# Optimization experiments

Hardware: AMD Instinct MI355X
Metric: run time of the kernel (lower is better)

The kernel has to match this reference:

```python
import jax, jax.numpy as jnp
import numpy as np
from jax import lax

B, H, W = 32, 30, 30          # batch of ARC-style grids (max 30x30)
D, NH = 256, 4                # hidden_dim, num_heads (ARPSConfig)
L, P = 8, 12                  # max_program_length, number of primitives
NUM_COLORS = 10
PAINT_COLOR = 3


def setup_inputs() -> dict:
    key = jax.random.key(0)
    ks = jax.random.split(key, 11)
    s = 0.02
    return {
        "grid": jax.random.randint(ks[0], (B, H, W), 0, NUM_COLORS, dtype=jnp.int32),
        "anchor": jax.random.randint(ks[1], (B, 2), 0, min(H, W), dtype=jnp.int32),
        "embed": jax.random.normal(ks[2], (NUM_COLORS, D), jnp.float32) * s,
        "pos_emb": jax.random.normal(ks[3], (H * W, D), jnp.float32) * s,
        "wq": jax.random.normal(ks[4], (D, D), jnp.float32) * s,
        "wk": jax.random.normal(ks[5], (D, D), jnp.float32) * s,
        "wv": jax.random.normal(ks[6], (D, D), jnp.float32) * s,
        "wo": jax.random.normal(ks[7], (D, D), jnp.float32) * s,
        "step_q": jax.random.normal(ks[8], (L, D), jnp.float32) * s,
        "w_out": jax.random.normal(ks[9], (D, P), jnp.float32) * s,
        "b_out": jnp.zeros((P,), jnp.float32),
    }


def _mha(q, k, v, nh):
    b, lq, d = q.shape
    hd = d // nh
    qh = q.reshape(b, lq, nh, hd)
    kh = k.reshape(b, k.shape[1], nh, hd)
    vh = v.reshape(b, v.shape[1], nh, hd)
    scores = jnp.einsum('bqhd,bkhd->bhqk', qh, kh) / jnp.sqrt(jnp.asarray(hd, q.dtype))
    attn = jax.nn.softmax(scores, axis=-1)
    return jnp.einsum('bhqk,bkhd->bqhd', attn, vh).reshape(b, lq, d)


def _execute_one(grid, anchor):
    """Fixed anchor-relative program: select_connected((0,0)) -> rotate_90 -> paint."""
    h, w = grid.shape
    ar = jnp.clip(anchor[0], 0, h - 1)
    ac = jnp.clip(anchor[1], 0, w - 1)
    # --- select_connected: 4-connected component of seed color (parallel flood fill) ---
    seed_color = grid[ar, ac]
    same = grid == seed_color
    m0 = jnp.zeros((h, w), bool).at[ar, ac].set(True)

    def dilate(m):
        p = jnp.pad(m, 1)
        return m | p[:-2, 1:-1] | p[2:, 1:-1] | p[1:-1, :-2] | p[1:-1, 2:]

    def body(st):
        m = st[0]
        nm = dilate(m) & same
        return (nm, jnp.any(nm != m))

    mask, _ = lax.while_loop(lambda st: st[1], body, (m0, jnp.array(True)))
    sel = mask.astype(jnp.float32)
    # --- rotate_90 clockwise around anchor: (dr,dc) -> (dc,-dr); out-of-bounds dropped ---
    rr = jnp.broadcast_to(jnp.arange(h)[:, None], (h, w))
    cc = jnp.broadcast_to(jnp.arange(w)[None, :], (h, w))
    nr = ar + (cc - ac)
    nc = ac - (rr - ar)
    rot = jnp.zeros_like(sel).at[nr, nc].set(sel, mode='drop')
    # --- paint: overwrite selected pixels with PAINT_COLOR ---
    return jnp.where(rot > 0.5, jnp.int32(PAINT_COLOR), grid)


def reference(grid, anchor, embed, pos_emb, wq, wk, wv, wo, step_q, w_out, b_out):
    b = grid.shape[0]
    tok = embed[grid.reshape(b, -1)] + pos_emb                  # (B, T=900, D)
    tok = tok + _mha(tok @ wq, tok @ wk, tok @ wv, NH) @ wo     # self-attn over pixels
    sq = jnp.broadcast_to(step_q, (b,) + step_q.shape)          # (B, L, D) step queries
    hsteps = _mha(sq @ wq, tok @ wk, tok @ wv, NH) @ wo         # cross-attn: steps -> pixels
    logits = hsteps @ w_out + b_out                             # (B, L, P) primitive logits
    out_grid = jax.vmap(_execute_one)(grid, anchor)             # (B, H, W) executed program
    return logits, out_grid
```

## Files before the change

kernel.cpp:

```cpp
#include <hip/hip_runtime.h>


typedef __attribute__((ext_vector_type(8))) short bf16x8;
typedef __attribute__((ext_vector_type(4))) float f32x4;

constexpr float kScl = 0.18033688011112042f;

__device__ __forceinline__ short f2bf(float f) {
  union { float f; unsigned u; } v; v.f = f;
  unsigned r = v.u + 0x7fffu + ((v.u >> 16) & 1u);
  return (short)(r >> 16);
}
__device__ __forceinline__ float bf2f(short s) {
  union { unsigned u; float f; } v; v.u = ((unsigned)(unsigned short)s) << 16;
  return v.f;
}
__device__ __forceinline__ unsigned cvt_pk_bf16(float lo, float hi) {
  unsigned r;
  asm("v_cvt_pk_bf16_f32 %0, %1, %2" : "=v"(r) : "v"(lo), "v"(hi));
  return r;
}
__device__ __forceinline__ float exp2f_fast(float x) {
  return __builtin_amdgcn_exp2f(x);
}
__device__ __forceinline__ int swz(int row, int col) {
  return row * 64 + ((((col >> 3) ^ row) & 7) << 3) + (col & 7);
}
__device__ __forceinline__ int a256(int row, int col) {
  return row * 256 + (col & ~63) + (((((col >> 3) & 7) ^ row) & 7) << 3);
}
__device__ __forceinline__ void gload16(const short* gsrc, short* lds) {
  __builtin_amdgcn_global_load_lds(
      (const __attribute__((address_space(1))) unsigned int*)gsrc,
      (__attribute__((address_space(3))) unsigned int*)lds, 16, 0, 0);
}

constexpr size_t OFF_POSQ  = 0;
constexpr size_t OFF_POSK  = 230400;
constexpr size_t OFF_POSV  = 460800;
constexpr size_t OFF_EMBQ  = 691200;
constexpr size_t OFF_EMBK  = 693760;
constexpr size_t OFF_EMBV  = 696320;
constexpr size_t OFF_WOOUT = 698880;
constexpr size_t OFF_Q2    = 701952;
constexpr size_t OFF_QP    = 704000;
constexpr size_t OFF_QE    = OFF_QP + 28800;
constexpr size_t OFF_WVO   = OFF_QE + 512;
constexpr size_t OFF_Q2K   = OFF_WVO + 12288;
constexpr size_t OFF_F32_END = 769536;
constexpr size_t SOFF_WOKVT = 0;
constexpr size_t SOFF_ATTN  = 131072;
constexpr size_t SOFF_KB    = 7503872;
constexpr size_t SOFF_VT    = 14876672;
constexpr size_t SOFF_E     = SOFF_KB;
constexpr size_t SOFF_UPART = SOFF_KB + 983040;
constexpr size_t SOFF_VPART = SOFF_UPART + 2097152;

__global__ __launch_bounds__(256) void k_pre(const float* __restrict__ pos_emb,
                                             const float* __restrict__ embed,
                                             const float* __restrict__ wq,
                                             const float* __restrict__ wk,
                                             const float* __restrict__ wv,
                                             const float* __restrict__ wo,
                                             const float* __restrict__ step_q,
                                             const float* __restrict__ w_out,
                                             float* __restrict__ ws) {
  const int blk = blockIdx.x;
  const int tid = threadIdx.x;
  if (blk >= 212) {
    const int b2 = blk - 212;
    int job, base;
    if      (b2 < 10) { job = 0; base = b2; }
    else if (b2 < 20) { job = 1; base = b2 - 10; }
    else if (b2 < 30) { job = 2; base = b2 - 20; }
    else if (b2 < 42) { job = 3; base = b2 - 30; }
    else              { job = 4; base = b2 - 42; }
    const float* A; const float* Wm; float* C; int M; int N;
    switch (job) {
      case 0: A=embed;  Wm=wq;    C=ws+OFF_EMBQ;  M=10;  N=256; break;
      case 1: A=embed;  Wm=wk;    C=ws+OFF_EMBK;  M=10;  N=256; break;
      case 2: A=embed;  Wm=wv;    C=ws+OFF_EMBV;  M=10;  N=256; break;
      case 3: A=wo;     Wm=w_out; C=ws+OFF_WOOUT; M=256; N=12;  break;
      default:A=step_q; Wm=wq;    C=ws+OFF_Q2;    M=8;   N=256; break;
    }
    int idx = base * 256 + tid;
    if (idx >= M * N) return;
    int m = idx / N, n = idx - m * N;
    const float* a = A + (size_t)m * 256;
    float acc = 0.f;
    #pragma unroll 8
    for (int k = 0; k < 256; ++k) acc = fmaf(a[k], Wm[(size_t)k * N + n], acc);
    C[idx] = acc;
    return;
  }

  bool wojob; int mt, n0, base_n = 0;
  const float* A; const float* W; float* C = nullptr;
  if (blk < 180) {
    wojob = false; mt = blk % 15; int nt = blk / 15;
    A = pos_emb;
    W = nt < 4 ? wq : (nt < 8 ? wk : wv);
    C = ws + (nt < 4 ? OFF_POSQ : (nt < 8 ? OFF_POSK : OFF_POSV));
    n0 = (nt & 3) * 64;
  } else {
    wojob = true; int j = blk - 180; mt = j & 3; int nt2 = j >> 2;
    A = wo;
    W = nt2 < 4 ? wk : wv;
    base_n = nt2 < 4 ? 0 : 256;
    n0 = (nt2 & 3) * 64;
  }
  const int m0 = mt * 64;
  const int tr = tid >> 4, tc = tid & 15;
  __shared__ float As[64][68];
  __shared__ float Bs[64][68];
  float acc[4][4] = {};
  for (int kc = 0; kc < 4; ++kc) {
    __syncthreads();
    for (int i = tid; i < 1024; i += 256) {
      int row = i >> 4, c4 = (i & 15) * 4;
      int m = m0 + row; if (m > 899) m = 899;
      *(float4*)&As[row][c4] = *(const float4*)&A[(size_t)m * 256 + kc * 64 + c4];
      *(float4*)&Bs[row][c4] = *(const float4*)&W[(size_t)(kc * 64 + row) * 256 + n0 + c4];
    }
    __syncthreads();
    #pragma unroll 8
    for (int kk = 0; kk < 64; ++kk) {
      float a0 = As[4*tr+0][kk], a1 = As[4*tr+1][kk];
      float a2 = As[4*tr+2][kk], a3 = As[4*tr+3][kk];
      float4 b4 = *(const float4*)&Bs[kk][4*tc];
      acc[0][0]+=a0*b4.x; acc[0][1]+=a0*b4.y; acc[0][2]+=a0*b4.z; acc[0][3]+=a0*b4.w;
      acc[1][0]+=a1*b4.x; acc[1][1]+=a1*b4.y; acc[1][2]+=a1*b4.z; acc[1][3]+=a1*b4.w;
      acc[2][0]+=a2*b4.x; acc[2][1]+=a2*b4.y; acc[2][2]+=a2*b4.z; acc[2][3]+=a2*b4.w;
      acc[3][0]+=a3*b4.x; acc[3][1]+=a3*b4.y; acc[3][2]+=a3*b4.z; acc[3][3]+=a3*b4.w;
    }
  }
  if (!wojob) {
    #pragma unroll
    for (int i = 0; i < 4; ++i) {
      int m = m0 + 4 * tr + i;
      if (m < 900)
        *(float4*)&C[(size_t)m * 256 + n0 + 4 * tc] =
            make_float4(acc[i][0], acc[i][1], acc[i][2], acc[i][3]);
    }
  } else {
    __syncthreads();
    #pragma unroll
    for (int i = 0; i < 4; ++i)
      #pragma unroll
      for (int j = 0; j < 4; ++j)
        Bs[4 * tc + j][4 * tr + i] = acc[i][j];
    __syncthreads();
    short* wokvT = (short*)(ws + OFF_F32_END) + SOFF_WOKVT;
    for (int i = tid; i < 512; i += 256) {
      int row = i >> 3, ch = i & 7;
      union { short s[8]; bf16x8 v; } u;
      #pragma unroll
      for (int jj = 0; jj < 8; ++jj) u.s[jj] = f2bf(Bs[row][ch * 8 + jj]);
      *(bf16x8*)&wokvT[(size_t)(base_n + n0 + row) * 256 + m0 + ch * 8] = u.v;
    }
  }
}

__global__ __launch_bounds__(256) void k_pre2(float* __restrict__ ws) {
  const float* q2 = ws + OFF_Q2;
  const short* wokvT = (const short*)(ws + OFF_F32_END) + SOFF_WOKVT;
  const int blk = blockIdx.x, tid = threadIdx.x;
  if (blk < 32) {
    int lh = blk, h = lh >> 3, l = lh & 7;
    __shared__ float qs[64];
    if (tid < 64) qs[tid] = q2[l * 256 + h * 64 + tid];
    __syncthreads();
    float acc = 0.f;
    for (int dd = 0; dd < 64; ++dd)
      acc = fmaf(qs[dd], bf2f(wokvT[(size_t)(h * 64 + dd) * 256 + tid]), acc);
    ((short*)(ws + OFF_Q2K))[lh * 256 + tid] = f2bf(acc);
  } else if (blk < 64) {
    int lh = blk - 32, h = lh >> 3, l = lh & 7;
    __shared__ float qs[64];
    if (tid < 64) qs[tid] = q2[l * 256 + h * 64 + tid];
    __syncthreads();
    const float* posK = ws + OFF_POSK;
    for (int t = tid; t < 900; t += 256) {
      float acc = 0.f;
      const float* pr = posK + (size_t)t * 256 + h * 64;
      #pragma unroll 8
      for (int dd = 0; dd < 64; ++dd) acc = fmaf(qs[dd], pr[dd], acc);
      ws[OFF_QP + (size_t)lh * 900 + t] = acc;
    }
  } else if (blk == 64) {
    const float* embK = ws + OFF_EMBK;
    if (tid < 320) {
      int lh = tid / 10, c = tid - lh * 10;
      int h = lh >> 3, l = lh & 7;
      float acc = 0.f;
      const float* qrow = q2 + l * 256 + h * 64;
      const float* er = embK + (size_t)c * 256 + h * 64;
      for (int dd = 0; dd < 64; ++dd) acc = fmaf(qrow[dd], er[dd], acc);
      ws[OFF_QE + lh * 16 + c] = acc;
    }
  } else {
    int h = blk - 65;
    const float* woOut = ws + OFF_WOOUT;
    __shared__ float wos[64][12];
    for (int i = tid; i < 768; i += 256) wos[i / 12][i % 12] = woOut[(h * 64 + i / 12) * 12 + i % 12];
    __syncthreads();
    float acc[12] = {};
    for (int dd = 0; dd < 64; ++dd) {
      float v = bf2f(wokvT[(size_t)(256 + h * 64 + dd) * 256 + tid]);
      #pragma unroll
      for (int p = 0; p < 12; ++p) acc[p] = fmaf(v, wos[dd][p], acc[p]);
    }
    #pragma unroll
    for (int p = 0; p < 12; ++p)
      ws[OFF_WVO + ((size_t)h * 256 + tid) * 12 + p] = acc[p];
  }
}

__global__ __launch_bounds__(256) void k_kv(const int* __restrict__ grid_in,
                                            const float* __restrict__ ws,
                                            short* __restrict__ Kb,
                                            short* __restrict__ VT) {
  const int kt = blockIdx.x, b = blockIdx.y;
  const int t0 = kt * 64, tid = threadIdx.x;
  const float* posK = ws + OFF_POSK;
  const float* embK = ws + OFF_EMBK;
  const float* posV = ws + OFF_POSV;
  const float* embV = ws + OFF_EMBV;

  for (int i = tid; i < 2048; i += 256) {
    int row = i >> 5, ch = i & 31;
    int t = t0 + row;
    if (t > 899) continue;
    int g = grid_in[b * 900 + t];
    const float* pk = posK + (size_t)t * 256 + ch * 8;
    const float* ek = embK + (size_t)g * 256 + ch * 8;
    float4 p0 = *(const float4*)pk, p1 = *(const float4*)(pk + 4);
    float4 e0 = *(const float4*)ek, e1 = *(const float4*)(ek + 4);
    union { short s[8]; bf16x8 v; } u;
    u.s[0] = f2bf(p0.x + e0.x); u.s[1] = f2bf(p0.y + e0.y);
    u.s[2] = f2bf(p0.z + e0.z); u.s[3] = f2bf(p0.w + e0.w);
    u.s[4] = f2bf(p1.x + e1.x); u.s[5] = f2bf(p1.y + e1.y);
    u.s[6] = f2bf(p1.z + e1.z); u.s[7] = f2bf(p1.w + e1.w);
    *(bf16x8*)&Kb[((size_t)(b * 900 + t)) * 256 + ch * 8] = u.v;
  }

  __shared__ float Lf[64 * 65];
  for (int h = 0; h < 4; ++h) {
    __syncthreads();
    for (int i = tid; i < 512; i += 256) {
      int row = i >> 3, ch = i & 7;
      int t = t0 + row; if (t > 899) t = 899;
      int g = grid_in[b * 900 + t];
      const float* pv = posV + (size_t)t * 256 + h * 64 + ch * 8;
      const float* ev = embV + (size_t)g * 256 + h * 64 + ch * 8;
      float4 p0 = *(const float4*)pv, p1 = *(const float4*)(pv + 4);
      float4 e0 = *(const float4*)ev, e1 = *(const float4*)(ev + 4);
      float* L = &Lf[row * 65 + ch * 8];
      L[0] = p0.x + e0.x; L[1] = p0.y + e0.y; L[2] = p0.z + e0.z; L[3] = p0.w + e0.w;
      L[4] = p1.x + e1.x; L[5] = p1.y + e1.y; L[6] = p1.z + e1.z; L[7] = p1.w + e1.w;
    }
    __syncthreads();
    short* tile = VT + ((size_t)((b * 4 + h) * 15 + kt)) * 4096;
    #pragma unroll
    for (int u = 0; u < 2; ++u) {
      int unit = u * 256 + tid;
      int d = unit >> 3;
      int t8 = (unit & 7) * 8;
      union { short s[8]; bf16x8 v; } p;
      #pragma unroll
      for (int i = 0; i < 8; ++i) p.s[i] = f2bf(Lf[(t8 + i) * 65 + d]);
      *(bf16x8*)&tile[d * 64 + t8] = p.v;
    }
  }
}

__global__ __launch_bounds__(256) void k_attn(const int* __restrict__ grid_in,
                                              const float* __restrict__ ws,
                                              const short* __restrict__ Kb,
                                              const short* __restrict__ VT,
                                              short* __restrict__ attnOut) {
  const int bidx = blockIdx.x;
  const int bh = ((bidx >> 6) << 3) | (bidx & 7);
  const int qt = (bidx >> 3) & 7;
  const int h = bh & 3, b = bh >> 2;
  const int t0 = qt * 128, hc = h * 64;
  const int tid = threadIdx.x, w = tid >> 6, lane = tid & 63;
  const int g = lane >> 4, c16 = lane & 15;
  const size_t tileBase = (size_t)(bh * 15) * 4096;

  __shared__ __align__(16) short Ks[2][4096];
  __shared__ __align__(16) short Vs[2][4096];
  __shared__ __align__(16) short Ps[4096];

  const float* posQ = ws + OFF_POSQ;
  const float* embQ = ws + OFF_EMBQ;

  bf16x8 aQ[2][2];
  #pragma unroll
  for (int s = 0; s < 2; ++s) {
    int t = t0 + s * 64 + w * 16 + c16; if (t > 899) t = 899;
    int gq = grid_in[b * 900 + t];
    #pragma unroll
    for (int kc = 0; kc < 2; ++kc) {
      union { short s8[8]; bf16x8 v; } u;
      #pragma unroll
      for (int j = 0; j < 8; ++j) {
        int d = hc + kc * 32 + g * 8 + j;
        u.s8[j] = f2bf(kScl * (embQ[gq * 256 + d] + posQ[(size_t)t * 256 + d]));
      }
      aQ[s][kc] = u.v;
    }
  }

#define STAGE(BUF, KT)                                                        \
  do {                                                                        \
    int kk0_ = (KT) * 64;                                                     \
    _Pragma("unroll")                                                         \
    for (int j_ = 0; j_ < 2; ++j_) {                                          \
      int c_ = j_ * 256 + w * 64 + lane;                                      \
      int row_ = c_ >> 3, ch_ = c_ & 7;                                       \
      int t_ = kk0_ + row_; if (t_ > 899) t_ = 899;                           \
      int sw_ = ((ch_ ^ row_) & 7) << 3;                                      \
      gload16(Kb + ((size_t)(b * 900 + t_)) * 256 + hc + sw_,                 \
              &Ks[BUF][(j_ * 256 + w * 64) << 3]);                            \
      gload16(VT + tileBase + (size_t)(KT) * 4096 + (row_ << 6) + sw_,        \
              &Vs[BUF][(j_ * 256 + w * 64) << 3]);                            \
    }                                                                         \
  } while (0)

  float l_[2] = {0.f, 0.f};
  f32x4 O[2][4];
  #pragma unroll
  for (int s = 0; s < 2; ++s)
    #pragma unroll
    for (int dt = 0; dt < 4; ++dt) { f32x4 z = {0.f,0.f,0.f,0.f}; O[s][dt] = z; }

  STAGE(0, 0);
  __syncthreads();

  int cur = 0;
  for (int kt = 0; kt < 15; ++kt) {
    if (kt + 1 < 15) STAGE(cur ^ 1, kt + 1);

    if (kt < 14) {
      f32x4 sacc[2][4];
      #pragma unroll
      for (int ct = 0; ct < 4; ++ct) {
        bf16x8 aK0 = *(bf16x8*)&Ks[cur][swz(ct * 16 + c16, g * 8)];
        bf16x8 aK1 = *(bf16x8*)&Ks[cur][swz(ct * 16 + c16, 32 + g * 8)];
        #pragma unroll
        for (int s = 0; s < 2; ++s) {
          f32x4 z = {0.f, 0.f, 0.f, 0.f};
          z = __builtin_amdgcn_mfma_f32_16x16x32_bf16(aK0, aQ[s][0], z, 0, 0, 0);
          z = __builtin_amdgcn_mfma_f32_16x16x32_bf16(aK1, aQ[s][1], z, 0, 0, 0);
          sacc[s][ct] = z;
        }
      }
      #pragma unroll
      for (int s = 0; s < 2; ++s) {
        float rs = 0.f;
        unsigned pk[4][2];
        #pragma unroll
        for (int ct = 0; ct < 4; ++ct) {
          float p0 = exp2f_fast(sacc[s][ct][0]);
          float p1 = exp2f_fast(sacc[s][ct][1]);
          float p2 = exp2f_fast(sacc[s][ct][2]);
          float p3 = exp2f_fast(sacc[s][ct][3]);
          rs += (p0 + p1) + (p2 + p3);
          pk[ct][0] = cvt_pk_bf16(p0, p1);
          pk[ct][1] = cvt_pk_bf16(p2, p3);
        }
        rs += __shfl_xor(rs, 16);
        rs += __shfl_xor(rs, 32);
        l_[s] += rs;
        #pragma unroll
        for (int ct = 0; ct < 4; ++ct)
          *(uint2*)&Ps[swz(w * 16 + c16, ct * 16 + 4 * g)] =
              make_uint2(pk[ct][0], pk[ct][1]);
        #pragma unroll
        for (int c = 0; c < 2; ++c) {
          bf16x8 aP = *(bf16x8*)&Ps[swz(w * 16 + c16, c * 32 + g * 8)];
          #pragma unroll
          for (int dt = 0; dt < 4; ++dt) {
            bf16x8 bV = *(bf16x8*)&Vs[cur][swz(dt * 16 + c16, c * 32 + g * 8)];
            O[s][dt] = __builtin_amdgcn_mfma_f32_16x16x32_bf16(aP, bV, O[s][dt], 0, 0, 0);
          }
        }
      }
    } else {
      bf16x8 aK0 = *(bf16x8*)&Ks[cur][swz(c16, g * 8)];
      bf16x8 aK1 = *(bf16x8*)&Ks[cur][swz(c16, 32 + g * 8)];
      #pragma unroll
      for (int s = 0; s < 2; ++s) {
        f32x4 z = {0.f, 0.f, 0.f, 0.f};
        z = __builtin_amdgcn_mfma_f32_16x16x32_bf16(aK0, aQ[s][0], z, 0, 0, 0);
        z = __builtin_amdgcn_mfma_f32_16x16x32_bf16(aK1, aQ[s][1], z, 0, 0, 0);
        float p0 = 0.f, p1 = 0.f, p2 = 0.f, p3 = 0.f;
        if (g == 0) {
          p0 = exp2f_fast(z[0]); p1 = exp2f_fast(z[1]);
          p2 = exp2f_fast(z[2]); p3 = exp2f_fast(z[3]);
        }
        float rs = (p0 + p1) + (p2 + p3);
        rs += __shfl_xor(rs, 16);
        rs += __shfl_xor(rs, 32);
        l_[s] += rs;
        *(uint2*)&Ps[swz(w * 16 + c16, 4 * g)] =
            make_uint2(cvt_pk_bf16(p0, p1), cvt_pk_bf16(p2, p3));
        *(uint2*)&Ps[swz(w * 16 + c16, 16 + 4 * g)] = make_uint2(0u, 0u);
        bf16x8 aP = *(bf16x8*)&Ps[swz(w * 16 + c16, g * 8)];
        #pragma unroll
        for (int dt = 0; dt < 4; ++dt) {
          bf16x8 bV = *(bf16x8*)&Vs[cur][swz(dt * 16 + c16, g * 8)];
          O[s][dt] = __builtin_amdgcn_mfma_f32_16x16x32_bf16(aP, bV, O[s][dt], 0, 0, 0);
        }
      }
    }

    __syncthreads();
    cur ^= 1;
  }
#undef STAGE

  #pragma unroll
  for (int s = 0; s < 2; ++s) {
    #pragma unroll
    for (int r = 0; r < 4; ++r) {
      float lq = __shfl(l_[s], (g << 4) | (4 * g + r));
      int t = t0 + s * 64 + w * 16 + 4 * g + r;
      if (t < 900) {
        float inv = 1.f / lq;
        #pragma unroll
        for (int dt = 0; dt < 4; ++dt)
          attnOut[((size_t)(b * 900 + t)) * 256 + hc + dt * 16 + c16] =
              f2bf(O[s][dt][r] * inv);
      }
    }
  }
}

__global__ __launch_bounds__(256) void k_crossA(const int* __restrict__ grid_in,
                                                const float* __restrict__ ws,
                                                const short* __restrict__ attnOut,
                                                short* __restrict__ E,
                                                float* __restrict__ Sp) {
  const int kt = blockIdx.x, b = blockIdx.y;
  const int t0 = kt * 64;
  const int tid = threadIdx.x, w = tid >> 6, lane = tid & 63;
  const int g = lane >> 4, c16 = lane & 15;
  __shared__ __align__(16) short Aat[16384];
  __shared__ __align__(16) short Qk[8192];
  __shared__ float qpL[32 * 72];
  __shared__ float qeL[512];
  __shared__ int   gtl[64];
  __shared__ float spW[128];

  #pragma unroll
  for (int it = 0; it < 8; ++it) {
    int idx = it * 256 + w * 64 + lane;
    int row = idx >> 5, ch = idx & 31;
    int t = t0 + row; if (t > 899) t = 899;
    int sw = (((ch & 7) ^ row) & 7) << 3;
    gload16(attnOut + ((size_t)(b * 900 + t)) * 256 + (ch >> 3) * 64 + sw,
            &Aat[(it * 256 + w * 64) << 3]);
  }
  const short* q2k = (const short*)(ws + OFF_Q2K);
  #pragma unroll
  for (int it = 0; it < 4; ++it) {
    int idx = it * 256 + w * 64 + lane;
    int row = idx >> 5, ch = idx & 31;
    int sw = (((ch & 7) ^ row) & 7) << 3;
    gload16(q2k + (size_t)row * 256 + (ch >> 3) * 64 + sw,
            &Qk[(it * 256 + w * 64) << 3]);
  }
  #pragma unroll
  for (int it = 0; it < 2; ++it) {
    int idx = it * 256 + tid, row = idx >> 4, c4 = (idx & 15) * 4;
    *(float4*)&qpL[row * 72 + c4] = *(const float4*)&ws[OFF_QP + (size_t)row * 900 + t0 + c4];
  }
  for (int idx = tid; idx < 512; idx += 256) qeL[idx] = ws[OFF_QE + idx];
  if (tid < 64) { int t = t0 + tid; gtl[tid] = grid_in[b * 900 + (t > 899 ? 899 : t)]; }
  __syncthreads();

  f32x4 sacc[2];
  { f32x4 z = {0.f,0.f,0.f,0.f}; sacc[0] = z; sacc[1] = z; }
  #pragma unroll
  for (int kk = 0; kk < 8; ++kk) {
    bf16x8 aA = *(bf16x8*)&Aat[a256(w * 16 + c16, kk * 32 + g * 8)];
    bf16x8 b0 = *(bf16x8*)&Qk[a256(c16, kk * 32 + g * 8)];
    bf16x8 b1 = *(bf16x8*)&Qk[a256(16 + c16, kk * 32 + g * 8)];
    sacc[0] = __builtin_amdgcn_mfma_f32_16x16x32_bf16(aA, b0, sacc[0], 0, 0, 0);
    sacc[1] = __builtin_amdgcn_mfma_f32_16x16x32_bf16(aA, b1, sacc[1], 0, 0, 0);
  }
  #pragma unroll
  for (int ct = 0; ct < 2; ++ct) {
    int lh = ct * 16 + c16;
    float e[4]; float rs = 0.f;
    #pragma unroll
    for (int r = 0; r < 4; ++r) {
      int tl = w * 16 + g * 4 + r;
      float s = kScl * (sacc[ct][r] + qpL[lh * 72 + tl] + qeL[lh * 16 + gtl[tl]]);
      e[r] = (t0 + tl < 900) ? exp2f_fast(s) : 0.f;
      rs += e[r];
    }
    *(uint2*)&E[((size_t)(b * 32 + lh)) * 960 + t0 + w * 16 + g * 4] =
        make_uint2(cvt_pk_bf16(e[0], e[1]), cvt_pk_bf16(e[2], e[3]));
    rs += __shfl_xor(rs, 16);
    rs += __shfl_xor(rs, 32);
    if (g == 0) spW[w * 32 + lh] = rs;
  }
  __syncthreads();
  if (tid < 32)
    Sp[((size_t)b * 32 + tid) * 15 + kt] =
        spW[tid] + spW[32 + tid] + spW[64 + tid] + spW[96 + tid];
}

__global__ __launch_bounds__(256) void k_crossP(const short* __restrict__ attnOut,
                                                const short* __restrict__ E,
                                                const short* __restrict__ VT,
                                                short* __restrict__ Upart,
                                                short* __restrict__ Vpart) {
  const int ktg = blockIdx.x, b = blockIdx.y;
  const int tid = threadIdx.x, w = tid >> 6, lane = tid & 63;
  const int g = lane >> 4, c16 = lane & 15;
  const int h = w, ctv = h >> 1;
  __shared__ __align__(16) short AT[256 * 72];
  __shared__ __align__(16) short Et[2048];
  __shared__ __align__(16) short VTl[16384];

  f32x4 Uacc[2][4], Vacc[4];
  { f32x4 z = {0.f,0.f,0.f,0.f};
    #pragma unroll
    for (int a = 0; a < 2; ++a)
      #pragma unroll
      for (int q = 0; q < 4; ++q) Uacc[a][q] = z;
    #pragma unroll
    for (int a = 0; a < 4; ++a) Vacc[a] = z; }

  const int ntile = (ktg < 7) ? 2 : 1;
  for (int tt = 0; tt < ntile; ++tt) {
    const int kt = ktg * 2 + tt, t0 = kt * 64;
    if (tt) __syncthreads();
    #pragma unroll
    for (int it = 0; it < 8; ++it) {
      int idx = it * 256 + tid;
      int tl = idx >> 5, jc = idx & 31;
      int t = t0 + tl; if (t > 899) t = 899;
      bf16x8 v = *(const bf16x8*)&attnOut[((size_t)(b * 900 + t)) * 256 + jc * 8];
      #pragma unroll
      for (int ii = 0; ii < 8; ++ii)
        AT[(jc * 8 + ii) * 72 + ((((tl >> 3) ^ jc) & 7) << 3) + (tl & 7)] = v[ii];
    }
    {
      int idx = w * 64 + lane;
      int row = idx >> 3, ch = idx & 7;
      int sw = ((ch ^ row) & 7) << 3;
      gload16(E + ((size_t)(b * 32 + row)) * 960 + t0 + sw, &Et[(w * 64) << 3]);
    }
    #pragma unroll
    for (int it = 0; it < 8; ++it) {
      int idx = it * 256 + w * 64 + lane;
      int hh = idx >> 9, rem = idx & 511;
      int row = rem >> 3, ch = rem & 7;
      int sw = ((ch ^ row) & 7) << 3;
      gload16(VT + ((size_t)((b * 4 + hh) * 15 + kt)) * 4096 + row * 64 + sw,
              &VTl[(it * 256 + w * 64) << 3]);
    }
    __syncthreads();
    #pragma unroll
    for (int kk = 0; kk < 2; ++kk) {
      bf16x8 aE0 = *(bf16x8*)&Et[swz(c16, kk * 32 + g * 8)];
      bf16x8 aE1 = *(bf16x8*)&Et[swz(16 + c16, kk * 32 + g * 8)];
      #pragma unroll
      for (int q = 0; q < 4; ++q) {
        int j = (w * 4 + q) * 16 + c16;
        int tch = kk * 4 + g;
        bf16x8 bA = *(bf16x8*)&AT[j * 72 + (((tch ^ (j >> 3)) & 7) << 3)];
        Uacc[0][q] = __builtin_amdgcn_mfma_f32_16x16x32_bf16(aE0, bA, Uacc[0][q], 0, 0, 0);
        Uacc[1][q] = __builtin_amdgcn_mfma_f32_16x16x32_bf16(aE1, bA, Uacc[1][q], 0, 0, 0);
      }
      bf16x8 bE = (ctv == 0) ? aE0 : aE1;
      #pragma unroll
      for (int rt = 0; rt < 4; ++rt) {
        bf16x8 aV = *(bf16x8*)&VTl[h * 4096 + swz(rt * 16 + c16, kk * 32 + g * 8)];
        Vacc[rt] = __builtin_amdgcn_mfma_f32_16x16x32_bf16(aV, bE, Vacc[rt], 0, 0, 0);
      }
    }
  }
  #pragma unroll
  for (int rt = 0; rt < 2; ++rt)
    #pragma unroll
    for (int q = 0; q < 4; ++q) {
      int j = (w * 4 + q) * 16 + c16;
      #pragma unroll
      for (int r = 0; r < 4; ++r) {
        int lh = rt * 16 + g * 4 + r;
        Upart[(((size_t)(ktg * 32 + b)) * 32 + lh) * 256 + j] = f2bf(Uacc[rt][q][r]);
      }
    }
  if ((c16 >> 3) == (h & 1)) {
    int l = c16 & 7;
    #pragma unroll
    for (int rt = 0; rt < 4; ++rt)
      #pragma unroll
      for (int r = 0; r < 4; ++r) {
        int d = rt * 16 + g * 4 + r;
        Vpart[((((size_t)(ktg * 32 + b)) * 4 + h) * 64 + d) * 8 + l] = f2bf(Vacc[rt][r]);
      }
  }
}

__global__ void k_crossR(const float* __restrict__ ws,
                         const float* __restrict__ b_out,
                         const short* __restrict__ Upart,
                         const short* __restrict__ Vpart,
                         const float* __restrict__ Sp,
                         float* __restrict__ out) {
  const int bl = blockIdx.x, b = bl >> 3, l = bl & 7;
  const int tid = threadIdx.x;
  __shared__ float Us[4][256];
  __shared__ float Vsm[4][64];
  __shared__ float Sinv[4];
  __shared__ float part[4][12];
  for (int h = 0; h < 4; ++h) {
    int lh = h * 8 + l;
    for (int j = tid; j < 256; j += 64) {
      float a = 0.f;
      #pragma unroll
      for (int kg = 0; kg < 8; ++kg)
        a += bf2f(Upart[(((size_t)(kg * 32 + b)) * 32 + lh) * 256 + j]);
      Us[h][j] = a;
    }
    float a = 0.f;
    #pragma unroll
    for (int kg = 0; kg < 8; ++kg)
      a += bf2f(Vpart[((((size_t)(kg * 32 + b)) * 4 + h) * 64 + tid) * 8 + l]);
    Vsm[h][tid] = a;
  }
  if (tid < 4) {
    int lh = tid * 8 + l;
    float s = 0.f;
    #pragma unroll
    for (int k = 0; k < 15; ++k) s += Sp[((size_t)b * 32 + lh) * 15 + k];
    Sinv[tid] = 1.f / s;
  }
  __syncthreads();
  if (tid < 48) {
    int h = tid / 12, p = tid % 12;
    const float* woOut = ws + OFF_WOOUT;
    const float* WVO = ws + OFF_WVO;
    float acc = 0.f;
    for (int dd = 0; dd < 64; ++dd)
      acc = fmaf(Vsm[h][dd], woOut[(h * 64 + dd) * 12 + p], acc);
    for (int j = 0; j < 256; ++j)
      acc = fmaf(Us[h][j], WVO[((size_t)h * 256 + j) * 12 + p], acc);
    part[h][p] = acc * Sinv[h];
  }
  __syncthreads();
  if (tid < 12)
    out[(size_t)bl * 12 + tid] =
        b_out[tid] + part[0][tid] + part[1][tid] + part[2][tid] + part[3][tid];
}

__global__ void k_execute(const int* __restrict__ grid_in,
                          const int* __restrict__ anchor,
                          float* __restrict__ outg) {
  const int b = blockIdx.x;
  const int lane = threadIdx.x;
  const int* g = grid_in + b * 900;
  int ar = anchor[2 * b], ac = anchor[2 * b + 1];
  ar = min(max(ar, 0), 29); ac = min(max(ac, 0), 29);
  const int seed = g[ar * 30 + ac];

  unsigned same = 0u;
  if (lane < 30)
    for (int c = 0; c < 30; ++c) same |= (unsigned)(g[lane * 30 + c] == seed) << c;

  unsigned cur = (lane == ar) ? (1u << ac) : 0u;
  bool changed = true;
  while (changed) {
    unsigned up = __shfl(cur, (lane + 63) & 63);
    unsigned dn = __shfl(cur, (lane + 1) & 63);
    if (lane == 0) up = 0u;
    unsigned nm = (cur | (cur << 1) | (cur >> 1) | up | dn) & same;
    changed = __any(nm != cur);
    cur = nm;
  }

  __shared__ unsigned msh[32];
  if (lane < 32) msh[lane] = (lane < 30) ? cur : 0u;
  __syncthreads();

  if (lane < 30) {
    unsigned rot = 0u;
    int cc = lane - ar + ac;
    if (cc >= 0 && cc < 30) {
      for (int nc = 0; nc < 30; ++nc) {
        int rr = ar + ac - nc;
        if (rr >= 0 && rr < 30) rot |= ((msh[rr] >> cc) & 1u) << nc;
      }
    }
    for (int c = 0; c < 30; ++c) {
      int v = ((rot >> c) & 1u) ? 3 : g[lane * 30 + c];
      outg[b * 900 + lane * 30 + c] = (float)v;
    }
  }
}

extern "C" void kernel_launch(void* const* d_in, const int* in_sizes, int n_in,
                              void* d_out, int out_size, void* d_ws, size_t ws_size,
                              hipStream_t stream) {
  const int*   grid_in = (const int*)d_in[0];
  const int*   anchor  = (const int*)d_in[1];
  const float* embed   = (const float*)d_in[2];
  const float* pos_emb = (const float*)d_in[3];
  const float* wq      = (const float*)d_in[4];
  const float* wk      = (const float*)d_in[5];
  const float* wv      = (const float*)d_in[6];
  const float* wo      = (const float*)d_in[7];
  const float* step_q  = (const float*)d_in[8];
  const float* w_out   = (const float*)d_in[9];
  const float* b_out   = (const float*)d_in[10];
  float* out = (float*)d_out;
  float* ws  = (float*)d_ws;
  short* wsS = (short*)(ws + OFF_F32_END);

  k_pre<<<dim3(262), dim3(256), 0, stream>>>(pos_emb, embed, wq, wk, wv, wo,
                                             step_q, w_out, ws);
  k_pre2<<<dim3(69), dim3(256), 0, stream>>>(ws);
  k_kv<<<dim3(15, 32), dim3(256), 0, stream>>>(grid_in, ws,
                                               wsS + SOFF_KB, wsS + SOFF_VT);
  k_attn<<<dim3(1024), dim3(256), 0, stream>>>(grid_in, ws, wsS + SOFF_KB,
                                               wsS + SOFF_VT, wsS + SOFF_ATTN);
  short* E  = wsS + SOFF_E;
  float* Sp = (float*)(wsS + SOFF_WOKVT);
  k_crossA<<<dim3(15, 32), dim3(256), 0, stream>>>(grid_in, ws, wsS + SOFF_ATTN, E, Sp);
  k_crossP<<<dim3(8, 32), dim3(256), 0, stream>>>(wsS + SOFF_ATTN, E, wsS + SOFF_VT,
                                                  wsS + SOFF_UPART, wsS + SOFF_VPART);
  k_crossR<<<dim3(256), dim3(64), 0, stream>>>(ws, b_out, wsS + SOFF_UPART,
                                               wsS + SOFF_VPART, Sp, out);
  k_execute<<<dim3(32), dim3(64), 0, stream>>>(grid_in, anchor, out + 32 * 8 * 12);
}
```

Before: 226.6 us.

## Merge launches for pre2/kv and crossR/execute; batch PV MFMAs with priority hints

```diff
diff --git a/kernel.cpp b/kernel.cpp
--- a/kernel.cpp
+++ b/kernel.cpp
@@ -161,67 +161,72 @@
   }
 }
 
-__global__ __launch_bounds__(256) void k_pre2(float* __restrict__ ws) {
-  const float* q2 = ws + OFF_Q2;
-  const short* wokvT = (const short*)(ws + OFF_F32_END) + SOFF_WOKVT;
+__global__ __launch_bounds__(256) void k_kvp(const int* __restrict__ grid_in,
+                                             float* __restrict__ ws,
+                                             short* __restrict__ Kb,
+                                             short* __restrict__ VT) {
   const int blk = blockIdx.x, tid = threadIdx.x;
-  if (blk < 32) {
-    int lh = blk, h = lh >> 3, l = lh & 7;
-    __shared__ float qs[64];
-    if (tid < 64) qs[tid] = q2[l * 256 + h * 64 + tid];
-    __syncthreads();
-    float acc = 0.f;
-    for (int dd = 0; dd < 64; ++dd)
-      acc = fmaf(qs[dd], bf2f(wokvT[(size_t)(h * 64 + dd) * 256 + tid]), acc);
-    ((short*)(ws + OFF_Q2K))[lh * 256 + tid] = f2bf(acc);
-  } else if (blk < 64) {
-    int lh = blk - 32, h = lh >> 3, l = lh & 7;
-    __shared__ float qs[64];
-    if (tid < 64) qs[tid] = q2[l * 256 + h * 64 + tid];
-    __syncthreads();
-    const float* posK = ws + OFF_POSK;
-    for (int t = tid; t < 900; t += 256) {
+  __shared__ float Lf[64 * 65];
+
+  if (blk >= 480) {
+    const int b2 = blk - 480;
+    const float* q2 = ws + OFF_Q2;
+    const short* wokvT = (const short*)(ws + OFF_F32_END) + SOFF_WOKVT;
+    if (b2 < 32) {
+      int lh = b2, h = lh >> 3, l = lh & 7;
+      float* qs = Lf;
+      if (tid < 64) qs[tid] = q2[l * 256 + h * 64 + tid];
+      __syncthreads();
       float acc = 0.f;
-      const float* pr = posK + (size_t)t * 256 + h * 64;
-      #pragma unroll 8
-      for (int dd = 0; dd < 64; ++dd) acc = fmaf(qs[dd], pr[dd], acc);
-      ws[OFF_QP + (size_t)lh * 900 + t] = acc;
-    }
-  } else if (blk == 64) {
-    const float* embK = ws + OFF_EMBK;
-    if (tid < 320) {
-      int lh = tid / 10, c = tid - lh * 10;
-      int h = lh >> 3, l = lh & 7;
-      float acc = 0.f;
-      const float* qrow = q2 + l * 256 + h * 64;
-      const float* er = embK + (size_t)c * 256 + h * 64;
-      for (int dd = 0; dd < 64; ++dd) acc = fmaf(qrow[dd], er[dd], acc);
-      ws[OFF_QE + lh * 16 + c] = acc;
-    }
-  } else {
-    int h = blk - 65;
-    const float* woOut = ws + OFF_WOOUT;
-    __shared__ float wos[64][12];
-    for (int i = tid; i < 768; i += 256) wos[i / 12][i % 12] = woOut[(h * 64 + i / 12) * 12 + i % 12];
-    __syncthreads();
-    float acc[12] = {};
-    for (int dd = 0; dd < 64; ++dd) {
-      float v = bf2f(wokvT[(size_t)(256 + h * 64 + dd) * 256 + tid]);
-      #pragma unroll
-      for (int p = 0; p < 12; ++p) acc[p] = fmaf(v, wos[dd][p], acc[p]);
-    }
-    #pragma unroll
-    for (int p = 0; p < 12; ++p)
-      ws[OFF_WVO + ((size_t)h * 256 + tid) * 12 + p] = acc[p];
-  }
-}
-
-__global__ __launch_bounds__(256) void k_kv(const int* __restrict__ grid_in,
-                                            const float* __restrict__ ws,
-                                            short* __restrict__ Kb,
-                                            short* __restrict__ VT) {
-  const int kt = blockIdx.x, b = blockIdx.y;
-  const int t0 = kt * 64, tid = threadIdx.x;
+      for (int dd = 0; dd < 64; ++dd)
+        acc = fmaf(qs[dd], bf2f(wokvT[(size_t)(h * 64 + dd) * 256 + tid]), acc);
+      ((short*)(ws + OFF_Q2K))[lh * 256 + tid] = f2bf(acc);
+    } else if (b2 < 64) {
+      int lh = b2 - 32, h = lh >> 3, l = lh & 7;
+      float* qs = Lf;
+      if (tid < 64) qs[tid] = q2[l * 256 + h * 64 + tid];
+      __syncthreads();
+      const float* posK = ws + OFF_POSK;
+      for (int t = tid; t < 900; t += 256) {
+        float acc = 0.f;
+        const float* pr = posK + (size_t)t * 256 + h * 64;
+        #pragma unroll 8
+        for (int dd = 0; dd < 64; ++dd) acc = fmaf(qs[dd], pr[dd], acc);
+        ws[OFF_QP + (size_t)lh * 900 + t] = acc;
+      }
+    } else if (b2 == 64) {
+      const float* embK = ws + OFF_EMBK;
+      if (tid < 320) {
+        int lh = tid / 10, c = tid - lh * 10;
+        int h = lh >> 3, l = lh & 7;
+        float acc = 0.f;
+        const float* qrow = q2 + l * 256 + h * 64;
+        const float* er = embK + (size_t)c * 256 + h * 64;
+        for (int dd = 0; dd < 64; ++dd) acc = fmaf(qrow[dd], er[dd], acc);
+        ws[OFF_QE + lh * 16 + c] = acc;
+      }
+    } else {
+      int h = b2 - 65;
+      const float* woOut = ws + OFF_WOOUT;
+      float (*wos)[12] = (float(*)[12])Lf;
+      for (int i = tid; i < 768; i += 256)
+        wos[i / 12][i % 12] = woOut[(h * 64 + i / 12) * 12 + i % 12];
+      __syncthreads();
+      float acc[12] = {};
+      for (int dd = 0; dd < 64; ++dd) {
+        float v = bf2f(wokvT[(size_t)(256 + h * 64 + dd) * 256 + tid]);
+        #pragma unroll
+        for (int p = 0; p < 12; ++p) acc[p] = fmaf(v, wos[dd][p], acc[p]);
+      }
+      #pragma unroll
+      for (int p = 0; p < 12; ++p)
+        ws[OFF_WVO + ((size_t)h * 256 + tid) * 12 + p] = acc[p];
+    }
+    return;
+  }
+
+  const int kt = blk % 15, b = blk / 15;
+  const int t0 = kt * 64;
   const float* posK = ws + OFF_POSK;
   const float* embK = ws + OFF_EMBK;
   const float* posV = ws + OFF_POSV;
@@ -244,7 +249,6 @@
     *(bf16x8*)&Kb[((size_t)(b * 900 + t)) * 256 + ch * 8] = u.v;
   }
 
-  __shared__ float Lf[64 * 65];
   for (int h = 0; h < 4; ++h) {
     __syncthreads();
     for (int i = tid; i < 512; i += 256) {
@@ -290,7 +294,7 @@
 
   __shared__ __align__(16) short Ks[2][4096];
   __shared__ __align__(16) short Vs[2][4096];
-  __shared__ __align__(16) short Ps[4096];
+  __shared__ __align__(16) short Ps[2][4096];
 
   const float* posQ = ws + OFF_POSQ;
   const float* embQ = ws + OFF_EMBQ;
@@ -344,6 +348,7 @@
 
     if (kt < 14) {
       f32x4 sacc[2][4];
+      __builtin_amdgcn_s_setprio(1);
       #pragma unroll
       for (int ct = 0; ct < 4; ++ct) {
         bf16x8 aK0 = *(bf16x8*)&Ks[cur][swz(ct * 16 + c16, g * 8)];
@@ -356,6 +361,7 @@
           sacc[s][ct] = z;
         }
       }
+      __builtin_amdgcn_s_setprio(0);
       #pragma unroll
       for (int s = 0; s < 2; ++s) {
         float rs = 0.f;
@@ -375,18 +381,22 @@
         l_[s] += rs;
         #pragma unroll
         for (int ct = 0; ct < 4; ++ct)
-          *(uint2*)&Ps[swz(w * 16 + c16, ct * 16 + 4 * g)] =
+          *(uint2*)&Ps[s][swz(w * 16 + c16, ct * 16 + 4 * g)] =
               make_uint2(pk[ct][0], pk[ct][1]);
+      }
+      __builtin_amdgcn_s_setprio(1);
+      #pragma unroll
+      for (int c = 0; c < 2; ++c) {
+        bf16x8 aP0 = *(bf16x8*)&Ps[0][swz(w * 16 + c16, c * 32 + g * 8)];
+        bf16x8 aP1 = *(bf16x8*)&Ps[1][swz(w * 16 + c16, c * 32 + g * 8)];
         #pragma unroll
-        for (int c = 0; c < 2; ++c) {
-          bf16x8 aP = *(bf16x8*)&Ps[swz(w * 16 + c16, c * 32 + g * 8)];
-          #pragma unroll
-          for (int dt = 0; dt < 4; ++dt) {
-            bf16x8 bV = *(bf16x8*)&Vs[cur][swz(dt * 16 + c16, c * 32 + g * 8)];
-            O[s][dt] = __builtin_amdgcn_mfma_f32_16x16x32_bf16(aP, bV, O[s][dt], 0, 0, 0);
-          }
+        for (int dt = 0; dt < 4; ++dt) {
+          bf16x8 bV = *(bf16x8*)&Vs[cur][swz(dt * 16 + c16, c * 32 + g * 8)];
+          O[0][dt] = __builtin_amdgcn_mfma_f32_16x16x32_bf16(aP0, bV, O[0][dt], 0, 0, 0);
+          O[1][dt] = __builtin_amdgcn_mfma_f32_16x16x32_bf16(aP1, bV, O[1][dt], 0, 0, 0);
         }
       }
+      __builtin_amdgcn_s_setprio(0);
     } else {
       bf16x8 aK0 = *(bf16x8*)&Ks[cur][swz(c16, g * 8)];
       bf16x8 aK1 = *(bf16x8*)&Ks[cur][swz(c16, 32 + g * 8)];
@@ -404,15 +414,17 @@
         rs += __shfl_xor(rs, 16);
         rs += __shfl_xor(rs, 32);
         l_[s] += rs;
-        *(uint2*)&Ps[swz(w * 16 + c16, 4 * g)] =
+        *(uint2*)&Ps[s][swz(w * 16 + c16, 4 * g)] =
             make_uint2(cvt_pk_bf16(p0, p1), cvt_pk_bf16(p2, p3));
-        *(uint2*)&Ps[swz(w * 16 + c16, 16 + 4 * g)] = make_uint2(0u, 0u);
-        bf16x8 aP = *(bf16x8*)&Ps[swz(w * 16 + c16, g * 8)];
-        #pragma unroll
-        for (int dt = 0; dt < 4; ++dt) {
-          bf16x8 bV = *(bf16x8*)&Vs[cur][swz(dt * 16 + c16, g * 8)];
-          O[s][dt] = __builtin_amdgcn_mfma_f32_16x16x32_bf16(aP, bV, O[s][dt], 0, 0, 0);
-        }
+        *(uint2*)&Ps[s][swz(w * 16 + c16, 16 + 4 * g)] = make_uint2(0u, 0u);
+      }
+      bf16x8 aP0 = *(bf16x8*)&Ps[0][swz(w * 16 + c16, g * 8)];
+      bf16x8 aP1 = *(bf16x8*)&Ps[1][swz(w * 16 + c16, g * 8)];
+      #pragma unroll
+      for (int dt = 0; dt < 4; ++dt) {
+        bf16x8 bV = *(bf16x8*)&Vs[cur][swz(dt * 16 + c16, g * 8)];
+        O[0][dt] = __builtin_amdgcn_mfma_f32_16x16x32_bf16(aP0, bV, O[0][dt], 0, 0, 0);
+        O[1][dt] = __builtin_amdgcn_mfma_f32_16x16x32_bf16(aP1, bV, O[1][dt], 0, 0, 0);
       }
     }
 
@@ -609,18 +621,66 @@
   }
 }
 
-__global__ void k_crossR(const float* __restrict__ ws,
-                         const float* __restrict__ b_out,
-                         const short* __restrict__ Upart,
-                         const short* __restrict__ Vpart,
-                         const float* __restrict__ Sp,
-                         float* __restrict__ out) {
-  const int bl = blockIdx.x, b = bl >> 3, l = bl & 7;
+__global__ void k_tail(const float* __restrict__ ws,
+                       const float* __restrict__ b_out,
+                       const short* __restrict__ Upart,
+                       const short* __restrict__ Vpart,
+                       const float* __restrict__ Sp,
+                       const int* __restrict__ grid_in,
+                       const int* __restrict__ anchor,
+                       float* __restrict__ out) {
   const int tid = threadIdx.x;
   __shared__ float Us[4][256];
   __shared__ float Vsm[4][64];
   __shared__ float Sinv[4];
   __shared__ float part[4][12];
+  __shared__ unsigned msh[32];
+
+  if (blockIdx.x >= 256) {
+    const int b = blockIdx.x - 256;
+    const int lane = tid;
+    const int* g = grid_in + b * 900;
+    float* outg = out + 32 * 8 * 12;
+    int ar = anchor[2 * b], ac = anchor[2 * b + 1];
+    ar = min(max(ar, 0), 29); ac = min(max(ac, 0), 29);
+    const int seed = g[ar * 30 + ac];
+
+    unsigned same = 0u;
+    if (lane < 30)
+      for (int c = 0; c < 30; ++c) same |= (unsigned)(g[lane * 30 + c] == seed) << c;
+
+    unsigned cur = (lane == ar) ? (1u << ac) : 0u;
+    bool changed = true;
+    while (changed) {
+      unsigned up = __shfl(cur, (lane + 63) & 63);
+      unsigned dn = __shfl(cur, (lane + 1) & 63);
+      if (lane == 0) up = 0u;
+      unsigned nm = (cur | (cur << 1) | (cur >> 1) | up | dn) & same;
+      changed = __any(nm != cur);
+      cur = nm;
+    }
+
+    if (lane < 32) msh[lane] = (lane < 30) ? cur : 0u;
+    __syncthreads();
+
+    if (lane < 30) {
+      unsigned rot = 0u;
+      int cc = lane - ar + ac;
+      if (cc >= 0 && cc < 30) {
+        for (int nc = 0; nc < 30; ++nc) {
+          int rr = ar + ac - nc;
+          if (rr >= 0 && rr < 30) rot |= ((msh[rr] >> cc) & 1u) << nc;
+        }
+      }
+      for (int c = 0; c < 30; ++c) {
+        int v = ((rot >> c) & 1u) ? 3 : g[lane * 30 + c];
+        outg[b * 900 + lane * 30 + c] = (float)v;
+      }
+    }
+    return;
+  }
+
+  const int bl = blockIdx.x, b = bl >> 3, l = bl & 7;
   for (int h = 0; h < 4; ++h) {
     int lh = h * 8 + l;
     for (int j = tid; j < 256; j += 64) {
@@ -659,51 +719,6 @@
   if (tid < 12)
     out[(size_t)bl * 12 + tid] =
         b_out[tid] + part[0][tid] + part[1][tid] + part[2][tid] + part[3][tid];
-}
-
-__global__ void k_execute(const int* __restrict__ grid_in,
-                          const int* __restrict__ anchor,
-                          float* __restrict__ outg) {
-  const int b = blockIdx.x;
-  const int lane = threadIdx.x;
-  const int* g = grid_in + b * 900;
-  int ar = anchor[2 * b], ac = anchor[2 * b + 1];
-  ar = min(max(ar, 0), 29); ac = min(max(ac, 0), 29);
-  const int seed = g[ar * 30 + ac];
-
-  unsigned same = 0u;
-  if (lane < 30)
-    for (int c = 0; c < 30; ++c) same |= (unsigned)(g[lane * 30 + c] == seed) << c;
-
-  unsigned cur = (lane == ar) ? (1u << ac) : 0u;
-  bool changed = true;
-  while (changed) {
-    unsigned up = __shfl(cur, (lane + 63) & 63);
-    unsigned dn = __shfl(cur, (lane + 1) & 63);
-    if (lane == 0) up = 0u;
-    unsigned nm = (cur | (cur << 1) | (cur >> 1) | up | dn) & same;
-    changed = __any(nm != cur);
-    cur = nm;
-  }
-
-  __shared__ unsigned msh[32];
-  if (lane < 32) msh[lane] = (lane < 30) ? cur : 0u;
-  __syncthreads();
-
-  if (lane < 30) {
-    unsigned rot = 0u;
-    int cc = lane - ar + ac;
-    if (cc >= 0 && cc < 30) {
-      for (int nc = 0; nc < 30; ++nc) {
-        int rr = ar + ac - nc;
-        if (rr >= 0 && rr < 30) rot |= ((msh[rr] >> cc) & 1u) << nc;
-      }
-    }
-    for (int c = 0; c < 30; ++c) {
-      int v = ((rot >> c) & 1u) ? 3 : g[lane * 30 + c];
-      outg[b * 900 + lane * 30 + c] = (float)v;
-    }
-  }
 }
 
 extern "C" void kernel_launch(void* const* d_in, const int* in_sizes, int n_in,
@@ -726,9 +741,8 @@
 
   k_pre<<<dim3(262), dim3(256), 0, stream>>>(pos_emb, embed, wq, wk, wv, wo,
                                              step_q, w_out, ws);
-  k_pre2<<<dim3(69), dim3(256), 0, stream>>>(ws);
-  k_kv<<<dim3(15, 32), dim3(256), 0, stream>>>(grid_in, ws,
-                                               wsS + SOFF_KB, wsS + SOFF_VT);
+  k_kvp<<<dim3(549), dim3(256), 0, stream>>>(grid_in, ws,
+                                             wsS + SOFF_KB, wsS + SOFF_VT);
   k_attn<<<dim3(1024), dim3(256), 0, stream>>>(grid_in, ws, wsS + SOFF_KB,
                                                wsS + SOFF_VT, wsS + SOFF_ATTN);
   short* E  = wsS + SOFF_E;
@@ -736,7 +750,6 @@
   k_crossA<<<dim3(15, 32), dim3(256), 0, stream>>>(grid_in, ws, wsS + SOFF_ATTN, E, Sp);
   k_crossP<<<dim3(8, 32), dim3(256), 0, stream>>>(wsS + SOFF_ATTN, E, wsS + SOFF_VT,
                                                   wsS + SOFF_UPART, wsS + SOFF_VPART);
-  k_crossR<<<dim3(256), dim3(64), 0, stream>>>(ws, b_out, wsS + SOFF_UPART,
-                                               wsS + SOFF_VPART, Sp, out);
-  k_execute<<<dim3(32), dim3(64), 0, stream>>>(grid_in, anchor, out + 32 * 8 * 12);
-}
+  k_tail<<<dim3(288), dim3(64), 0, stream>>>(ws, b_out, wsS + SOFF_UPART,
+                                             wsS + SOFF_VPART, Sp, grid_in, anchor, out);
+}
```

Measured after the change: 211.0 us. 6.9% less time.
